# Kernel tuning notes

Hardware: AMD Instinct MI355X
Metric: run time of the kernel (lower is better)

Reference implementation:

```python
import jax, jax.numpy as jnp
import numpy as np

DIM = 64
K = 8
B_TAIL = 3.0
HID = 128
BATCH = 131072
MIN_BIN_WIDTH = 1e-3
MIN_BIN_HEIGHT = 1e-3
MIN_DERIVATIVE = 1e-3


def setup_inputs() -> dict:
    key = jax.random.key(0)
    ks = jax.random.split(key, 9)
    nin = DIM // 2
    nout = (3 * K - 1) * (DIM - DIM // 2)
    dims = [nin, HID, HID, HID, nout]
    d = {"x": jax.random.normal(ks[0], (BATCH, DIM), jnp.float32)}
    for i in range(4):
        d[f"W{i+1}"] = jax.random.normal(ks[1 + 2 * i], (dims[i], dims[i + 1]), jnp.float32) / jnp.sqrt(dims[i])
        d[f"b{i+1}"] = jax.random.normal(ks[2 + 2 * i], (dims[i + 1],), jnp.float32) * 0.01
    return d


def _gather(a, idx):
    # a: [..., K or K+1], idx: [...] int -> [...]
    return jnp.take_along_axis(a, idx[..., None], axis=-1)[..., 0]


def _mlp(x, W1, b1, W2, b2, W3, b3, W4, b4):
    h = jax.nn.elu(x @ W1 + b1)
    h = jax.nn.elu(h @ W2 + b2)
    h = jax.nn.elu(h @ W3 + b3)
    return h @ W4 + b4


def _unconstrained_rqs_fwd(inputs, uw, uh, ud, tail_bound):
    # inputs: [B, D2]; uw/uh: [B, D2, K]; ud: [B, D2, K-1]
    num_bins = uw.shape[-1]
    left = bottom = -tail_bound
    right = top = tail_bound

    inside = (inputs >= -tail_bound) & (inputs <= tail_bound)
    x = jnp.clip(inputs, -tail_bound, tail_bound)  # safe values for spline math

    # pad derivatives and pin boundary slopes so spline matches identity tails
    const = float(np.log(np.exp(1.0 - MIN_DERIVATIVE) - 1.0))
    ud = jnp.pad(ud, [(0, 0)] * (ud.ndim - 1) + [(1, 1)], constant_values=const)

    widths = jax.nn.softmax(uw, axis=-1)
    widths = MIN_BIN_WIDTH + (1.0 - MIN_BIN_WIDTH * num_bins) * widths
    cumwidths = jnp.cumsum(widths, axis=-1)
    cumwidths = jnp.pad(cumwidths, [(0, 0)] * (cumwidths.ndim - 1) + [(1, 0)])
    cumwidths = (right - left) * cumwidths + left
    cumwidths = cumwidths.at[..., 0].set(left).at[..., -1].set(right)
    widths = cumwidths[..., 1:] - cumwidths[..., :-1]

    derivatives = MIN_DERIVATIVE + jax.nn.softplus(ud)

    heights = jax.nn.softmax(uh, axis=-1)
    heights = MIN_BIN_HEIGHT + (1.0 - MIN_BIN_HEIGHT * num_bins) * heights
    cumheights = jnp.cumsum(heights, axis=-1)
    cumheights = jnp.pad(cumheights, [(0, 0)] * (cumheights.ndim - 1) + [(1, 0)])
    cumheights = (top - bottom) * cumheights + bottom
    cumheights = cumheights.at[..., 0].set(bottom).at[..., -1].set(top)
    heights = cumheights[..., 1:] - cumheights[..., :-1]

    # searchsorted: number of bin edges <= x, minus one (eps on last edge)
    cw = cumwidths.at[..., -1].add(1e-6)
    bin_idx = jnp.sum((x[..., None] >= cw).astype(jnp.int32), axis=-1) - 1
    bin_idx = jnp.clip(bin_idx, 0, num_bins - 1)

    in_cw = _gather(cumwidths, bin_idx)
    in_w = _gather(widths, bin_idx)
    in_ch = _gather(cumheights, bin_idx)
    in_h = _gather(heights, bin_idx)
    delta = heights / widths
    in_delta = _gather(delta, bin_idx)
    in_d = _gather(derivatives, bin_idx)
    in_d1 = _gather(derivatives[..., 1:], bin_idx)

    theta = (x - in_cw) / in_w
    t1mt = theta * (1.0 - theta)
    numerator = in_h * (in_delta * theta ** 2 + in_d * t1mt)
    denominator = in_delta + (in_d + in_d1 - 2.0 * in_delta) * t1mt
    spline_out = in_ch + numerator / denominator
    deriv_num = in_delta ** 2 * (in_d1 * theta ** 2 + 2.0 * in_delta * t1mt + in_d * (1.0 - theta) ** 2)
    spline_ld = jnp.log(deriv_num) - 2.0 * jnp.log(denominator)

    outputs = jnp.where(inside, spline_out, inputs)
    logabsdet = jnp.where(inside, spline_ld, 0.0)
    return outputs, logabsdet


def reference(x, W1, b1, W2, b2, W3, b3, W4, b4):
    d_half = DIM // 2
    x1, x2 = x[:, :d_half], x[:, d_half:]
    out = _mlp(x1, W1, b1, W2, b2, W3, b3, W4, b4)
    out = out.reshape(-1, DIM - d_half, 3 * K - 1)
    W = out[..., :K]
    H = out[..., K:2 * K]
    D = out[..., 2 * K:]
    y2, ld = _unconstrained_rqs_fwd(x2, W, H, D, B_TAIL)
    log_det = jnp.sum(ld, axis=1)
    return jnp.concatenate([x1, y2], axis=1), log_det
```

## Files before the change

### kernel.cpp

```cpp
#include <hip/hip_runtime.h>
#include <hip/hip_bf16.h>
#include <math.h>

typedef _Float16 f16_t;
typedef _Float16 f16x4 __attribute__((ext_vector_type(4)));
typedef _Float16 f16x8 __attribute__((ext_vector_type(8)));
typedef float f32x4 __attribute__((ext_vector_type(4)));

#define BATCH 131072
#define MTILE 64
#define NBLK (BATCH / MTILE)
#define LOG2E 1.4426950408889634f

#define W1F 0
#define W2F 4096
#define W3F 20480
#define W4F 36864
#define B4S_OFF 67584

__global__ __launch_bounds__(256) void convert_weights_kernel(
    const float* __restrict__ W1, const float* __restrict__ W2,
    const float* __restrict__ W3, const float* __restrict__ W4,
    const float* __restrict__ b4, f16_t* __restrict__ wf,
    float* __restrict__ b4s) {
  int tid = blockIdx.x * 256 + threadIdx.x;
  if (tid >= 16896) {
    int i = tid - 16896;
    if (i < 736) {
      float s = ((i % 23) < 16) ? LOG2E : 1.f;
      b4s[i] = b4[i] * s;
    }
    return;
  }
  int lane = tid & 63;
  int l16 = lane & 15, lhi = lane >> 4;
  const float* W; int ncols, col, k0; bool zero = false; float scale = 1.f;
  if (tid < 512) {
    int n = tid >> 6;
    W = W1; ncols = 128; col = n * 16 + l16; k0 = lhi * 8;
  } else if (tid < 2560) {
    int g = tid - 512; int n = g >> 8, s = (g >> 6) & 3;
    W = W2; ncols = 128; col = n * 16 + l16; k0 = s * 32 + lhi * 8;
  } else if (tid < 4608) {
    int g = tid - 2560; int n = g >> 8, s = (g >> 6) & 3;
    W = W3; ncols = 128; col = n * 16 + l16; k0 = s * 32 + lhi * 8;
  } else {
    int g = tid - 4608; int t = g >> 8, s = (g >> 6) & 3;
    int c = t / 6, n = t - c * 6;
    int colc = n * 16 + l16;
    W = W4; ncols = 736; col = c * 92 + colc; k0 = s * 32 + lhi * 8;
    zero = (colc >= 92);
    if (!zero) scale = ((col % 23) < 16) ? LOG2E : 1.f;
  }
  f16x8 v;
#pragma unroll
  for (int j = 0; j < 8; ++j)
    v[j] = zero ? (f16_t)0.f : (f16_t)(W[(k0 + j) * ncols + col] * scale);
  *(f16x8*)(wf + (size_t)tid * 8) = v;
}

__device__ __forceinline__ float elu(float v) {
  return v > 0.f ? v : (__expf(v) - 1.f);
}

__device__ __forceinline__ void rqs_task(const f16_t* P, float xv,
                                         float& yout, float& ldout) {
  f16x8 pw = *(const f16x8*)P;
  f16x8 ph = *(const f16x8*)(P + 8);
  f16x8 pd = *(const f16x8*)(P + 16);

  float ew[8], sw = 0.f;
#pragma unroll
  for (int i = 0; i < 8; ++i) { ew[i] = exp2f((float)pw[i]); sw += ew[i]; }
  float invw = 0.992f * __builtin_amdgcn_rcpf(sw);
  float cw[8]; cw[0] = -3.f;
  float accw = 0.f;
#pragma unroll
  for (int i = 0; i < 7; ++i) {
    accw += 0.001f + ew[i] * invw;
    cw[i + 1] = -3.f + 6.f * accw;
  }

  float eh[8], sh = 0.f;
#pragma unroll
  for (int i = 0; i < 8; ++i) { eh[i] = exp2f((float)ph[i]); sh += eh[i]; }
  float invh = 0.992f * __builtin_amdgcn_rcpf(sh);
  float ch[8]; ch[0] = -3.f;
  float acch = 0.f;
#pragma unroll
  for (int i = 0; i < 7; ++i) {
    acch += 0.001f + eh[i] * invh;
    ch[i + 1] = -3.f + 6.f * acch;
  }

  float xc = fminf(fmaxf(xv, -3.f), 3.f);
  int bin = 0;
#pragma unroll
  for (int i = 1; i < 8; ++i) bin += (xc >= cw[i]) ? 1 : 0;

  float in_cw = cw[0], in_ch = ch[0];
  float ewsel = ew[0], ehsel = eh[0];
  float sd  = (float)pd[0];
  float sd1 = (float)pd[0];
#pragma unroll
  for (int i = 1; i < 8; ++i) {
    bool g = (bin >= i);
    in_cw = g ? cw[i] : in_cw;  in_ch = g ? ch[i] : in_ch;
    ewsel = g ? ew[i] : ewsel;  ehsel = g ? eh[i] : ehsel;
    sd    = g ? (float)pd[i - 1] : sd;
  }
#pragma unroll
  for (int i = 1; i < 7; ++i)
    sd1 = (bin >= i) ? (float)pd[i] : sd1;

  float in_w = fmaf(ewsel * invw, 6.f, 0.006f);
  float in_h = fmaf(ehsel * invh, 6.f, 0.006f);

  float spd  = fmaxf(sd,  0.f) + __logf(1.f + __expf(-fabsf(sd)));
  float spd1 = fmaxf(sd1, 0.f) + __logf(1.f + __expf(-fabsf(sd1)));
  float in_d  = (bin == 0) ? 1.f : 0.001f + spd;
  float in_d1 = (bin == 7) ? 1.f : 0.001f + spd1;

  float rw = __builtin_amdgcn_rcpf(in_w);
  float dlt = in_h * rw;
  float th = (xc - in_cw) * rw;
  float om = 1.f - th;
  float t1 = th * om;
  float num = in_h * (dlt * th * th + in_d * t1);
  float den = dlt + (in_d + in_d1 - 2.f * dlt) * t1;
  float rden = __builtin_amdgcn_rcpf(den);
  float yo = in_ch + num * rden;
  float dn = dlt * dlt * (in_d1 * th * th + 2.f * dlt * t1 + in_d * om * om);
  float ldv = __logf(dn * rden * rden);
  bool inside = (xv >= -3.f) && (xv <= 3.f);
  yout = inside ? yo : xv;
  ldout = inside ? ldv : 0.f;
}

__device__ __forceinline__ void mid_layer_ip(f16_t* hH,
                                             const f16_t* __restrict__ wseg,
                                             const float* __restrict__ bg,
                                             int wv, int l16, int lhi, int lane) {
  f16x8 a[4];
#pragma unroll
  for (int s = 0; s < 4; ++s)
    a[s] = *(const f16x8*)&hH[(wv * 16 + l16) * 136 + s * 32 + lhi * 8];
#pragma unroll
  for (int n = 0; n < 8; ++n) {
    f32x4 acc = {0.f, 0.f, 0.f, 0.f};
#pragma unroll
    for (int s = 0; s < 4; ++s) {
      f16x8 b = *(const f16x8*)(wseg + (size_t)((n * 4 + s) * 64 + lane) * 8);
      acc = __builtin_amdgcn_mfma_f32_16x16x32_f16(a[s], b, acc, 0, 0, 0);
    }
    float bias = bg[n * 16 + l16];
#pragma unroll
    for (int r = 0; r < 4; ++r)
      hH[(wv * 16 + lhi * 4 + r) * 136 + n * 16 + l16] =
          (f16_t)elu(acc[r] + bias);
  }
}

__global__ __launch_bounds__(256, 4) void nsf_fused_kernel(
    const float* __restrict__ x,
    const float* __restrict__ b1g, const float* __restrict__ b2g,
    const float* __restrict__ b3g, const float* __restrict__ b4s,
    const f16_t* __restrict__ wf,
    float* __restrict__ out) {
  __shared__ f16_t hH[MTILE * 136];
  __shared__ float x2s[MTILE * 33];

  const int tid = threadIdx.x;
  const int lane = tid & 63;
  const int wv = tid >> 6;
  const int l16 = lane & 15, lhi = lane >> 4;
  const int row0 = blockIdx.x * MTILE;

  {
    const float4* x4 = (const float4*)(x + (size_t)row0 * 64);
    float4* o4 = (float4*)(out + (size_t)row0 * 64);
#pragma unroll
    for (int it = 0; it < 4; ++it) {
      int idx = tid + it * 256;
      int row = idx >> 4, q = idx & 15;
      float4 v = x4[row * 16 + q];
      if (q < 8) {
        o4[row * 16 + q] = v;
        f16x4 p = {(f16_t)v.x, (f16_t)v.y, (f16_t)v.z, (f16_t)v.w};
        *(f16x4*)&hH[row * 136 + q * 4] = p;
      } else {
        int cb = row * 33 + (q - 8) * 4;
        x2s[cb + 0] = v.x; x2s[cb + 1] = v.y;
        x2s[cb + 2] = v.z; x2s[cb + 3] = v.w;
      }
    }
  }
  __syncthreads();

  {
    f16x8 a = *(const f16x8*)&hH[(wv * 16 + l16) * 136 + lhi * 8];
#pragma unroll
    for (int n = 0; n < 8; ++n) {
      f16x8 b = *(const f16x8*)(wf + W1F + (size_t)(n * 64 + lane) * 8);
      f32x4 acc = {0.f, 0.f, 0.f, 0.f};
      acc = __builtin_amdgcn_mfma_f32_16x16x32_f16(a, b, acc, 0, 0, 0);
      float bias = b1g[n * 16 + l16];
#pragma unroll
      for (int r = 0; r < 4; ++r)
        hH[(wv * 16 + lhi * 4 + r) * 136 + n * 16 + l16] =
            (f16_t)elu(acc[r] + bias);
    }
  }
  __syncthreads();

  mid_layer_ip(hH, wf + W2F, b2g, wv, l16, lhi, lane);
  __syncthreads();
  mid_layer_ip(hH, wf + W3F, b3g, wv, l16, lhi, lane);
  __syncthreads();

  {
    f16x8 a4[4];
#pragma unroll
    for (int s = 0; s < 4; ++s)
      a4[s] = *(const f16x8*)&hH[(wv * 16 + l16) * 136 + s * 32 + lhi * 8];
    __syncthreads();

    const int srow = tid >> 2;
    const int sjj = tid & 3;
    float ldp = 0.f;

    for (int c = 0; c < 8; ++c) {
#pragma unroll
      for (int n = 0; n < 6; ++n) {
        f32x4 acc = {0.f, 0.f, 0.f, 0.f};
#pragma unroll
        for (int s = 0; s < 4; ++s) {
          f16x8 b = *(const f16x8*)(wf + W4F +
                      (size_t)(((c * 6 + n) * 4 + s) * 64 + lane) * 8);
          acc = __builtin_amdgcn_mfma_f32_16x16x32_f16(a4[s], b, acc, 0, 0, 0);
        }
        int colc = n * 16 + l16;
        if (colc < 92) {
          int dm = (colc * 90) >> 11;
          int j = colc - dm * 23;
          float bias = b4s[c * 92 + colc];
#pragma unroll
          for (int r = 0; r < 4; ++r)
            hH[((wv * 16 + lhi * 4 + r) * 4 + dm) * 24 + j] =
                (f16_t)(acc[r] + bias);
        }
      }
      __builtin_amdgcn_wave_barrier();

      {
        int jg = c * 4 + sjj;
        float xv = x2s[srow * 33 + jg];
        float y0, l0;
        rqs_task(hH + tid * 24, xv, y0, l0);
        out[(size_t)(row0 + srow) * 64 + 32 + jg] = y0;
        ldp += l0;
      }
      __builtin_amdgcn_wave_barrier();
    }

    ldp += __shfl_xor(ldp, 1, 64);
    ldp += __shfl_xor(ldp, 2, 64);
    if ((tid & 3) == 0)
      out[(size_t)BATCH * 64 + row0 + srow] = ldp;
  }
}

extern "C" void kernel_launch(void* const* d_in, const int* in_sizes, int n_in,
                              void* d_out, int out_size, void* d_ws, size_t ws_size,
                              hipStream_t stream) {
  const float* x  = (const float*)d_in[0];
  const float* W1 = (const float*)d_in[1];
  const float* b1 = (const float*)d_in[2];
  const float* W2 = (const float*)d_in[3];
  const float* b2 = (const float*)d_in[4];
  const float* W3 = (const float*)d_in[5];
  const float* b3 = (const float*)d_in[6];
  const float* W4 = (const float*)d_in[7];
  const float* b4 = (const float*)d_in[8];
  f16_t* wf = (f16_t*)d_ws;
  float* b4s = (float*)d_ws + B4S_OFF;
  float* out = (float*)d_out;

  hipLaunchKernelGGL(convert_weights_kernel, dim3(69), dim3(256), 0, stream,
                     W1, W2, W3, W4, b4, wf, b4s);
  hipLaunchKernelGGL(nsf_fused_kernel, dim3(NBLK), dim3(256), 0, stream,
                     x, b1, b2, b3, b4s, wf, out);
}
```

Before: 98.09 us.

## Stage MLP weight slices cooperatively into shared memory per block

Each block now copies the f16 weight segments for every layer into a 16 KB LDS buffer in chunks, and the MFMA loops read B operands from LDS instead of each wave fetching them separately from global memory. The intent is to cut the four-fold redundant global/L2 weight traffic per block. In exchange it adds many block-wide barriers, with no overlap between the weight copies and the compute, and raises LDS use per block, which may limit occupancy. To save LDS, the x2 inputs are also stored as f16, which rounds both the spline inputs and the passthrough tail outputs and risks accuracy.

```diff
diff --git a/kernel.cpp b/kernel.cpp
--- a/kernel.cpp
+++ b/kernel.cpp
@@ -63,6 +63,13 @@
   return v > 0.f ? v : (__expf(v) - 1.f);
 }
 
+__device__ __forceinline__ void stage_w(f16_t* dst, const f16_t* __restrict__ src,
+                                        int nelem, int tid) {
+#pragma unroll
+  for (int k = tid * 8; k < nelem; k += 2048)
+    *(f16x8*)(dst + k) = *(const f16x8*)(src + k);
+}
+
 __device__ __forceinline__ void rqs_task(const f16_t* P, float xv,
                                          float& yout, float& ldout) {
   f16x8 pw = *(const f16x8*)P;
@@ -137,22 +144,19 @@
   ldout = inside ? ldv : 0.f;
 }
 
-__device__ __forceinline__ void mid_layer_ip(f16_t* hH,
-                                             const f16_t* __restrict__ wseg,
-                                             const float* __restrict__ bg,
-                                             int wv, int l16, int lhi, int lane) {
-  f16x8 a[4];
-#pragma unroll
-  for (int s = 0; s < 4; ++s)
-    a[s] = *(const f16x8*)&hH[(wv * 16 + l16) * 136 + s * 32 + lhi * 8];
-#pragma unroll
-  for (int n = 0; n < 8; ++n) {
+__device__ __forceinline__ void mid_half(f16_t* hH, const f16_t* wL,
+                                         const float* __restrict__ bg,
+                                         int nbase, const f16x8 a[4],
+                                         int wv, int l16, int lhi, int lane) {
+#pragma unroll
+  for (int nl = 0; nl < 4; ++nl) {
     f32x4 acc = {0.f, 0.f, 0.f, 0.f};
 #pragma unroll
     for (int s = 0; s < 4; ++s) {
-      f16x8 b = *(const f16x8*)(wseg + (size_t)((n * 4 + s) * 64 + lane) * 8);
+      f16x8 b = *(const f16x8*)(wL + (size_t)((nl * 4 + s) * 64 + lane) * 8);
       acc = __builtin_amdgcn_mfma_f32_16x16x32_f16(a[s], b, acc, 0, 0, 0);
     }
+    int n = nbase + nl;
     float bias = bg[n * 16 + l16];
 #pragma unroll
     for (int r = 0; r < 4; ++r)
@@ -168,7 +172,8 @@
     const f16_t* __restrict__ wf,
     float* __restrict__ out) {
   __shared__ f16_t hH[MTILE * 136];
-  __shared__ float x2s[MTILE * 33];
+  __shared__ f16_t wL[8192];
+  __shared__ f16_t x2s[MTILE * 32];
 
   const int tid = threadIdx.x;
   const int lane = tid & 63;
@@ -184,24 +189,23 @@
       int idx = tid + it * 256;
       int row = idx >> 4, q = idx & 15;
       float4 v = x4[row * 16 + q];
+      f16x4 p = {(f16_t)v.x, (f16_t)v.y, (f16_t)v.z, (f16_t)v.w};
       if (q < 8) {
         o4[row * 16 + q] = v;
-        f16x4 p = {(f16_t)v.x, (f16_t)v.y, (f16_t)v.z, (f16_t)v.w};
         *(f16x4*)&hH[row * 136 + q * 4] = p;
       } else {
-        int cb = row * 33 + (q - 8) * 4;
-        x2s[cb + 0] = v.x; x2s[cb + 1] = v.y;
-        x2s[cb + 2] = v.z; x2s[cb + 3] = v.w;
+        *(f16x4*)&x2s[row * 32 + (q - 8) * 4] = p;
       }
     }
   }
+  stage_w(wL, wf + W1F, 4096, tid);
   __syncthreads();
 
   {
     f16x8 a = *(const f16x8*)&hH[(wv * 16 + l16) * 136 + lhi * 8];
 #pragma unroll
     for (int n = 0; n < 8; ++n) {
-      f16x8 b = *(const f16x8*)(wf + W1F + (size_t)(n * 64 + lane) * 8);
+      f16x8 b = *(const f16x8*)(wL + (size_t)(n * 64 + lane) * 8);
       f32x4 acc = {0.f, 0.f, 0.f, 0.f};
       acc = __builtin_amdgcn_mfma_f32_16x16x32_f16(a, b, acc, 0, 0, 0);
       float bias = b1g[n * 16 + l16];
@@ -213,10 +217,23 @@
   }
   __syncthreads();
 
-  mid_layer_ip(hH, wf + W2F, b2g, wv, l16, lhi, lane);
-  __syncthreads();
-  mid_layer_ip(hH, wf + W3F, b3g, wv, l16, lhi, lane);
-  __syncthreads();
+#pragma unroll
+  for (int L = 0; L < 2; ++L) {
+    const f16_t* wseg = wf + (L ? W3F : W2F);
+    const float* bg = L ? b3g : b2g;
+    f16x8 a[4];
+#pragma unroll
+    for (int s = 0; s < 4; ++s)
+      a[s] = *(const f16x8*)&hH[(wv * 16 + l16) * 136 + s * 32 + lhi * 8];
+    stage_w(wL, wseg, 8192, tid);
+    __syncthreads();
+    mid_half(hH, wL, bg, 0, a, wv, l16, lhi, lane);
+    __syncthreads();
+    stage_w(wL, wseg + 8192, 8192, tid);
+    __syncthreads();
+    mid_half(hH, wL, bg, 4, a, wv, l16, lhi, lane);
+    __syncthreads();
+  }
 
   {
     f16x8 a4[4];
@@ -230,16 +247,38 @@
     float ldp = 0.f;
 
     for (int c = 0; c < 8; ++c) {
-#pragma unroll
-      for (int n = 0; n < 6; ++n) {
+      stage_w(wL, wf + W4F + (size_t)c * 12288, 8192, tid);
+      __syncthreads();
+#pragma unroll
+      for (int nl = 0; nl < 4; ++nl) {
         f32x4 acc = {0.f, 0.f, 0.f, 0.f};
 #pragma unroll
         for (int s = 0; s < 4; ++s) {
-          f16x8 b = *(const f16x8*)(wf + W4F +
-                      (size_t)(((c * 6 + n) * 4 + s) * 64 + lane) * 8);
+          f16x8 b = *(const f16x8*)(wL + (size_t)((nl * 4 + s) * 64 + lane) * 8);
           acc = __builtin_amdgcn_mfma_f32_16x16x32_f16(a4[s], b, acc, 0, 0, 0);
         }
-        int colc = n * 16 + l16;
+        int colc = nl * 16 + l16;
+        int dm = (colc * 90) >> 11;
+        int j = colc - dm * 23;
+        float bias = b4s[c * 92 + colc];
+#pragma unroll
+        for (int r = 0; r < 4; ++r)
+          hH[((wv * 16 + lhi * 4 + r) * 4 + dm) * 24 + j] =
+              (f16_t)(acc[r] + bias);
+      }
+      __syncthreads();
+
+      stage_w(wL, wf + W4F + (size_t)c * 12288 + 8192, 4096, tid);
+      __syncthreads();
+#pragma unroll
+      for (int nl = 0; nl < 2; ++nl) {
+        f32x4 acc = {0.f, 0.f, 0.f, 0.f};
+#pragma unroll
+        for (int s = 0; s < 4; ++s) {
+          f16x8 b = *(const f16x8*)(wL + (size_t)((nl * 4 + s) * 64 + lane) * 8);
+          acc = __builtin_amdgcn_mfma_f32_16x16x32_f16(a4[s], b, acc, 0, 0, 0);
+        }
+        int colc = (4 + nl) * 16 + l16;
         if (colc < 92) {
           int dm = (colc * 90) >> 11;
           int j = colc - dm * 23;
@@ -254,13 +293,13 @@
 
       {
         int jg = c * 4 + sjj;
-        float xv = x2s[srow * 33 + jg];
+        float xv = (float)x2s[srow * 32 + jg];
         float y0, l0;
         rqs_task(hH + tid * 24, xv, y0, l0);
         out[(size_t)(row0 + srow) * 64 + 32 + jg] = y0;
         ldp += l0;
       }
-      __builtin_amdgcn_wave_barrier();
+      __syncthreads();
     }
 
     ldp += __shfl_xor(ldp, 1, 64);
```

Result: slower. 101.5 us (+3.5%).
